# Kernel tuning notes

Measured on AMD Instinct MI355X. Metric: run time of the kernel, lower is better.

## Reference

```python
import jax, jax.numpy as jnp
import numpy as np

B = 64        # BATCH_SIZE
C_IN = 16
L = 8192
FFT0 = 64
FFT1 = 256
CO = 32       # c_out per fft branch (c_out=64 / 2 ffts)
RATIO = FFT1 // FFT0  # 4
EPS = 1e-5


def setup_inputs() -> dict:
    key = jax.random.key(0)
    ks = jax.random.split(key, 12)
    x = jax.random.normal(ks[0], (B, C_IN, L), jnp.float32)
    bn_gamma = 1.0 + 0.1 * jax.random.normal(ks[1], (2, B), jnp.float32)
    bn_beta = 0.1 * jax.random.normal(ks[2], (2, B), jnp.float32)
    mk_r = 0.1 * jax.random.normal(ks[3], (RATIO, RATIO), jnp.float32)
    mk_i = 0.1 * jax.random.normal(ks[4], (RATIO, RATIO), jnp.float32)
    mb_r = 0.1 * jax.random.normal(ks[5], (RATIO,), jnp.float32)
    mb_i = 0.1 * jax.random.normal(ks[6], (RATIO,), jnp.float32)
    fk0_r = 0.1 * jax.random.normal(ks[7], (FFT0 // 2 + 1, C_IN, CO), jnp.float32)
    fk0_i = 0.1 * jax.random.normal(ks[8], (FFT0 // 2 + 1, C_IN, CO), jnp.float32)
    fk1_r = 0.1 * jax.random.normal(ks[9], (FFT1 // 2 + 1, C_IN, CO), jnp.float32)
    fk1_i = 0.1 * jax.random.normal(ks[10], (FFT1 // 2 + 1, C_IN, CO), jnp.float32)
    pbias = 0.1 * jax.random.normal(ks[11], (2 * CO,), jnp.float32)
    return dict(x=x, bn_gamma=bn_gamma, bn_beta=bn_beta, mk_r=mk_r, mk_i=mk_i,
                mb_r=mb_r, mb_i=mb_i, fk0_r=fk0_r, fk0_i=fk0_i,
                fk1_r=fk1_r, fk1_i=fk1_i, pbias=pbias)


def _stft(x2d, n):
    # torch.stft(center=True, pad_mode='reflect', hop=n_fft, rect window),
    # then keep onesided bins and drop the last frame (as in the module).
    N = x2d.shape[0]
    xp = jnp.pad(x2d, ((0, 0), (n // 2, n // 2)), mode='reflect')
    frames = xp.reshape(N, -1, n)               # (N, T+1, n), hop == n_fft
    spec = jnp.fft.rfft(frames, axis=-1)        # onesided == [:, :, :n//2+1]
    return spec[:, :-1, :]                      # drop last frame -> (N, T, n//2+1)


def _zero_interp(p, ratio, out_f):
    # interleave (ratio-1) zeros along the freq axis, then crop to out_f bins
    b, t, f, c = p.shape
    z = jnp.zeros((b, t, f, ratio - 1, c), p.dtype)
    q = jnp.concatenate([p[:, :, :, None, :], z], axis=3).reshape(b, t, f * ratio, c)
    return q[:, :, :out_f, :]


def _cbn(xc, g, b):
    # BatchNorm2d(BATCH_SIZE) after permute(3,0,1,2): channel dim == batch dim,
    # stats over (c_in, T, F) per batch element; complex mean, |.|^2 variance.
    mu = jnp.mean(xc, axis=(1, 2, 3), keepdims=True)
    d = xc - mu
    var = jnp.mean((d * jnp.conj(d)).real, axis=(1, 2, 3), keepdims=True)
    xh = d / jnp.sqrt(var + EPS)
    return xh * g[:, None, None, None] + b[:, None, None, None]


def _istft(out, n):
    # out: (B, T, F, CO) complex. Mirrors permute/reshape + frame repeat + istft
    # (hop=n_fft, rect window, center=True -> trim n//2 on both ends).
    Bq, T, F, Co = out.shape
    pf = out.transpose(0, 3, 2, 1).reshape(Bq * Co, F, T)
    pf = jnp.concatenate([pf, pf[:, :, :1]], axis=-1)   # append copy of frame 0 -> T+1 frames
    fr = jnp.fft.irfft(pf, n=n, axis=1)                 # (N, n, T+1)
    sig = fr.transpose(0, 2, 1).reshape(Bq * Co, -1)    # overlap-add trivial (hop=n)
    sig = sig[:, n // 2: n // 2 + T * n]                # length L
    return sig.reshape(Bq, Co, -1).transpose(0, 2, 1)   # (B, L, CO)


def _forward(x, bn_gamma, bn_beta, mk_r, mk_i, mb_r, mb_i,
             fk0_r, fk0_i, fk1_r, fk1_i, pbias):
    x2 = x.reshape(B * C_IN, L)

    def spec(n):
        s = _stft(x2, n)                                 # (B*C_IN, T, n//2+1)
        T = s.shape[1]
        return s.reshape(B, C_IN, T, n // 2 + 1).transpose(0, 2, 3, 1)  # (B,T,F,C_IN)

    p0 = spec(FFT0)   # (B, 128, 33, 16)
    p1 = spec(FFT1)   # (B, 32, 129, 16)

    # attention merge across time (small fft -> large fft scale)
    pm = p0.reshape(B, -1, RATIO, FFT0 // 2 + 1, C_IN).transpose(0, 1, 3, 4, 2)  # (B,T1,F0,C,r)
    kc = mk_r + 1j * mk_i
    att = jnp.einsum('btfcr,rs->btfcs', pm, kc) + (mb_r + 1j * mb_i)
    a = jax.nn.softmax(jnp.abs(att), axis=-1)            # real weights (complex(a,0) in torch)
    merged = jnp.sum(pm * a, axis=-1) * float(RATIO)     # (B, T1, F0, C_IN)

    F1 = FFT1 // 2 + 1
    mask01 = _zero_interp(jnp.ones(merged.shape, jnp.float32), RATIO, F1)
    up = _zero_interp(merged, RATIO, F1)

    acc0 = p0                                            # own-scale mask is all ones
    acc1 = mask01 * up + (1.0 - mask01) * p1             # cross-scale + complementary mask

    def head(acc, g, b, fkr, fki, n):
        xbn = _cbn(acc, g, b)
        out = jnp.einsum('btfi,fio->btfo', xbn, fkr + 1j * fki)  # FILTER_FLAG merge
        return _istft(out, n)

    t0 = head(acc0, bn_gamma[0], bn_beta[0], fk0_r, fk0_i, FFT0)  # (B, L, CO)
    t1 = head(acc1, bn_gamma[1], bn_beta[1], fk1_r, fk1_i, FFT1)  # (B, L, CO)

    y = jnp.concatenate([t0, t1], axis=2) + pbias        # + patch_bias.real
    y = jax.nn.relu(y)                                   # ACT_DOMAIN == 'time'
    return y.transpose(0, 2, 1)                          # (B, c_out, L)


def reference(x, bn_gamma, bn_beta, mk_r, mk_i, mb_r, mb_i,
              fk0_r, fk0_i, fk1_r, fk1_i, pbias):
    return _forward(x, bn_gamma, bn_beta, mk_r, mk_i, mb_r, mb_i,
                    fk0_r, fk0_i, fk1_r, fk1_i, pbias)
```

## Files before the change

kernel.cpp:

```cpp
#include <hip/hip_runtime.h>
#include <math.h>

#define BB   64
#define CIN  16
#define LL   8192
#define CO   32
#define TCO  64
constexpr int T0n = 128;
constexpr int T1n = 32;
constexpr int F0n = 33;
constexpr int F1n = 129;

typedef unsigned int   uint32;
typedef unsigned short u16;
typedef __attribute__((ext_vector_type(8))) _Float16 half8;
typedef __attribute__((ext_vector_type(4))) float    f32x4;

template<int N, int F, int TFR, int NTILES, int KTT, int MT_W, int NT_W,
         int NT_STRIDE, bool MT_SPLIT>
__global__ __launch_bounds__(256)
void stft_mfma_kernel(const float* __restrict__ x,
                      const u16* __restrict__ dhi, const u16* __restrict__ dlo,
                      float* __restrict__ p) {
    constexpr int PADN = N + 8;
    __shared__ __align__(16) u16 Xhi[TFR * PADN];
    __shared__ __align__(16) u16 Xlo[TFR * PADN];
    int bc = blockIdx.x;
    const float* xrow = x + (size_t)bc * LL;

    for (int i = threadIdx.x; i < TFR * N; i += 256) {
        int row = i / N, colk = i % N;
        int gi = i - N / 2;
        gi = gi < 0 ? -gi : gi;
        float v = xrow[gi];
        _Float16 h = (_Float16)v;
        _Float16 l = (_Float16)(v - (float)h);
        Xhi[row * PADN + colk] = *(u16*)&h;
        Xlo[row * PADN + colk] = *(u16*)&l;
    }
    __syncthreads();

    int lane = threadIdx.x & 63, w = threadIdx.x >> 6;
    int col = lane & 15, quad = lane >> 4;
    f32x4 acc[MT_W][NT_W];
    #pragma unroll
    for (int mi = 0; mi < MT_W; ++mi)
        #pragma unroll
        for (int nj = 0; nj < NT_W; ++nj) {
            f32x4 z = {0.f, 0.f, 0.f, 0.f};
            acc[mi][nj] = z;
        }

    for (int kt = 0; kt < KTT; ++kt) {
        half8 ah[MT_W], al[MT_W];
        #pragma unroll
        for (int mi = 0; mi < MT_W; ++mi) {
            int mt = MT_SPLIT ? (w * MT_W + mi) : mi;
            int t  = mt * 16 + col;
            const u16* base = &Xhi[t * PADN + kt * 32 + quad * 8];
            ah[mi] = *(const half8*)base;
            al[mi] = *(const half8*)&Xlo[t * PADN + kt * 32 + quad * 8];
        }
        #pragma unroll
        for (int nj = 0; nj < NT_W; ++nj) {
            int nt = MT_SPLIT ? nj : (w + nj * NT_STRIDE);
            if (nt < NTILES) {
                half8 bh = ((const half8*)dhi)[(nt * KTT + kt) * 64 + lane];
                half8 bl = ((const half8*)dlo)[(nt * KTT + kt) * 64 + lane];
                #pragma unroll
                for (int mi = 0; mi < MT_W; ++mi) {
                    acc[mi][nj] = __builtin_amdgcn_mfma_f32_16x16x32_f16(ah[mi], bh, acc[mi][nj], 0, 0, 0);
                    acc[mi][nj] = __builtin_amdgcn_mfma_f32_16x16x32_f16(ah[mi], bl, acc[mi][nj], 0, 0, 0);
                    acc[mi][nj] = __builtin_amdgcn_mfma_f32_16x16x32_f16(al[mi], bh, acc[mi][nj], 0, 0, 0);
                }
            }
        }
    }

    int b = bc / CIN, c = bc % CIN;
    #pragma unroll
    for (int mi = 0; mi < MT_W; ++mi) {
        int mt = MT_SPLIT ? (w * MT_W + mi) : mi;
        #pragma unroll
        for (int nj = 0; nj < NT_W; ++nj) {
            int nt = MT_SPLIT ? nj : (w + nj * NT_STRIDE);
            if (nt < NTILES) {
                int j = nt * 16 + col;
                if (j < 2 * F) {
                    int t0 = mt * 16 + quad * 4;
                    f32x4 a = acc[mi][nj];
                    #pragma unroll
                    for (int r = 0; r < 4; ++r) {
                        p[(((size_t)b * TFR + t0 + r) * CIN + c) * (2 * F) + j] = a[r];
                    }
                }
            }
        }
    }
}

__global__ __launch_bounds__(256)
void init_d_kernel(u16* __restrict__ dhi0, u16* __restrict__ dlo0,
                   u16* __restrict__ dhi1, u16* __restrict__ dlo1) {
    int idx = blockIdx.x * 256 + threadIdx.x;
    constexpr int SZ0 = 5 * 2 * 64 * 8;
    constexpr int SZ1 = 17 * 8 * 64 * 8;
    int N, F, KTT, id; u16 *dh, *dl;
    if (idx < SZ0)            { N = 64;  F = F0n; KTT = 2; dh = dhi0; dl = dlo0; id = idx; }
    else if (idx < SZ0 + SZ1) { N = 256; F = F1n; KTT = 8; dh = dhi1; dl = dlo1; id = idx - SZ0; }
    else return;
    int jj   = id & 7;
    int lane = (id >> 3) & 63;
    int rest = id >> 9;
    int kt   = rest % KTT;
    int nt   = rest / KTT;
    int j = nt * 16 + (lane & 15);
    int k = kt * 32 + (lane >> 4) * 8 + jj;
    float v = 0.f;
    if (j < 2 * F) {
        int f = j >> 1;
        int u = (f * k) % N;
        double th = 6.283185307179586476925286766559 * (double)u / (double)N;
        v = (float)((j & 1) ? -sin(th) : cos(th));
    }
    _Float16 h = (_Float16)v;
    _Float16 l = (_Float16)(v - (float)h);
    dh[id] = *(u16*)&h;
    dl[id] = *(u16*)&l;
}

__global__ __launch_bounds__(256)
void merge_kernel(const float2* __restrict__ p0, float2* __restrict__ p1,
                  const float* __restrict__ mkr, const float* __restrict__ mki,
                  const float* __restrict__ mbr, const float* __restrict__ mbi) {
    int idx = blockIdx.x * 256 + threadIdx.x;
    const int total = BB * T1n * CIN * F0n;
    if (idx >= total) return;
    int f0 = idx % F0n; int r1 = idx / F0n;
    int c  = r1 % CIN;  int r2 = r1 / CIN;
    int t1 = r2 % T1n;  int b  = r2 / T1n;
    float2 pm[4];
    #pragma unroll
    for (int r = 0; r < 4; ++r) {
        int t = t1 * 4 + r;
        pm[r] = p0[(((size_t)b * T0n + t) * CIN + c) * F0n + f0];
    }
    float mag[4], mx = -1e30f;
    #pragma unroll
    for (int s = 0; s < 4; ++s) {
        float atr = mbr[s], ati = mbi[s];
        #pragma unroll
        for (int r = 0; r < 4; ++r) {
            float kr = mkr[r * 4 + s], ki = mki[r * 4 + s];
            atr = fmaf(pm[r].x, kr, atr); atr = fmaf(-pm[r].y, ki, atr);
            ati = fmaf(pm[r].x, ki, ati); ati = fmaf(pm[r].y, kr, ati);
        }
        mag[s] = sqrtf(atr * atr + ati * ati);
        mx = fmaxf(mx, mag[s]);
    }
    float se = 0.f;
    #pragma unroll
    for (int s = 0; s < 4; ++s) { mag[s] = expf(mag[s] - mx); se += mag[s]; }
    float inv = 4.0f / se;
    float mr = 0.f, mi = 0.f;
    #pragma unroll
    for (int r = 0; r < 4; ++r) { mr = fmaf(pm[r].x, mag[r], mr); mi = fmaf(pm[r].y, mag[r], mi); }
    p1[(((size_t)b * T1n + t1) * CIN + c) * F1n + 4 * f0] = make_float2(mr * inv, mi * inv);
}

__global__ __launch_bounds__(256)
void cbn_kernel(const float2* __restrict__ p0, const float2* __restrict__ p1,
                const float* __restrict__ gamma, const float* __restrict__ beta,
                float4* __restrict__ bn) {
    int head = blockIdx.x >> 6;
    int b    = blockIdx.x & 63;
    int Nel  = head ? (T1n * CIN * F1n) : (T0n * CIN * F0n);
    const float2* base = head ? (p1 + (size_t)b * (T1n * CIN * F1n))
                              : (p0 + (size_t)b * (T0n * CIN * F0n));
    float sr = 0.f, si = 0.f, s2 = 0.f;
    for (int i = threadIdx.x; i < Nel; i += 256) {
        float2 v = base[i];
        sr += v.x; si += v.y;
        s2 = fmaf(v.x, v.x, s2); s2 = fmaf(v.y, v.y, s2);
    }
    __shared__ float red[3][256];
    red[0][threadIdx.x] = sr; red[1][threadIdx.x] = si; red[2][threadIdx.x] = s2;
    __syncthreads();
    for (int off = 128; off > 0; off >>= 1) {
        if (threadIdx.x < off) {
            red[0][threadIdx.x] += red[0][threadIdx.x + off];
            red[1][threadIdx.x] += red[1][threadIdx.x + off];
            red[2][threadIdx.x] += red[2][threadIdx.x + off];
        }
        __syncthreads();
    }
    if (threadIdx.x == 0) {
        float invN = 1.f / (float)Nel;
        float mur = red[0][0] * invN, mui = red[1][0] * invN;
        float var = red[2][0] * invN - mur * mur - mui * mui;
        float g = gamma[head * BB + b] * rsqrtf(var + 1e-5f);
        bn[head * BB + b] = make_float4(g, beta[head * BB + b] - mur * g, -mui * g, 0.f);
    }
}

__global__ __launch_bounds__(256)
void init_w_kernel(u16* __restrict__ whi0, u16* __restrict__ wlo0,
                   u16* __restrict__ whi1, u16* __restrict__ wlo1) {
    int idx = blockIdx.x * 256 + threadIdx.x;
    int N, F, KT, id; u16 *dh, *dl;
    if (idx < 6144)              { N = 64;  F = F0n; KT = 3; dh = whi0; dl = wlo0; id = idx; }
    else if (idx < 6144 + 73728) { N = 256; F = F1n; KT = 9; dh = whi1; dl = wlo1; id = idx - 6144; }
    else return;
    int j    = id & 7;
    int lane = (id >> 3) & 63;
    int rest = id >> 9;
    int kt   = rest % KT;
    int mt   = rest / KT;
    int m  = mt * 16 + (lane & 15);
    int k2 = kt * 32 + (lane >> 4) * 8 + j;
    float v = 0.f;
    if (k2 < 2 * F) {
        int f = k2 >> 1;
        double scale = (f == 0 || f == F - 1) ? (1024.0 / N) : (2048.0 / N);
        int u = (m * f) % N;
        double th = 6.283185307179586476925286766559 * (double)u / (double)N;
        v = (float)((k2 & 1) ? (-scale * sin(th)) : (scale * cos(th)));
    }
    _Float16 h = (_Float16)v;
    _Float16 l = (_Float16)(v - (float)h);
    dh[id] = *(u16*)&h;
    dl[id] = *(u16*)&l;
}

__global__ __launch_bounds__(256)
void init_fk_kernel(const float* __restrict__ r0, const float* __restrict__ i0,
                    const float* __restrict__ r1, const float* __restrict__ i1,
                    float4* __restrict__ q0, float4* __restrict__ q1,
                    float2* __restrict__ s0, float2* __restrict__ s1) {
    int idx = blockIdx.x * 256 + threadIdx.x;
    constexpr int NQ0 = 8 * F0n * 32;
    constexpr int NQ1 = 8 * F1n * 32;
    constexpr int NS0 = F0n * 32;
    constexpr int NS1 = F1n * 32;
    if (idx < NQ0) {
        int id = idx;
        int c2 = id / (F0n * 32); int rem = id % (F0n * 32);
        int f = rem >> 5, o = rem & 31;
        int s = (f * CIN + 2 * c2) * CO + o;
        q0[id] = make_float4(r0[s], i0[s], r0[s + CO], i0[s + CO]);
    } else if (idx < NQ0 + NQ1) {
        int id = idx - NQ0;
        int c2 = id / (F1n * 32); int rem = id % (F1n * 32);
        int f = rem >> 5, o = rem & 31;
        int s = (f * CIN + 2 * c2) * CO + o;
        q1[id] = make_float4(r1[s], i1[s], r1[s + CO], i1[s + CO]);
    } else if (idx < NQ0 + NQ1 + NS0) {
        int id = idx - NQ0 - NQ1;
        int f = id >> 5, o = id & 31;
        float sr = 0.f, si = 0.f;
        for (int ci = 0; ci < CIN; ++ci) {
            int s = (f * CIN + ci) * CO + o;
            sr += r0[s]; si += i0[s];
        }
        s0[id] = make_float2(sr, si);
    } else if (idx < NQ0 + NQ1 + NS0 + NS1) {
        int id = idx - NQ0 - NQ1 - NS0;
        int f = id >> 5, o = id & 31;
        float sr = 0.f, si = 0.f;
        for (int ci = 0; ci < CIN; ++ci) {
            int s = (f * CIN + ci) * CO + o;
            sr += r1[s]; si += i1[s];
        }
        s1[id] = make_float2(sr, si);
    }
}

template<int N, int F, int TFR, int CH0, int KT, int KPAD>
__global__ __launch_bounds__(256)
void istft_kernel(const float2* __restrict__ p,
                  const u16* __restrict__ whi, const u16* __restrict__ wlo,
                  const float4* __restrict__ fkq, const float2* __restrict__ fks,
                  const float4* __restrict__ bn,
                  const float* __restrict__ pbias, float* __restrict__ out) {
    constexpr int MTW = N / 64;
    constexpr int FCO = F * CO;
    constexpr int QN  = (FCO + 255) / 256;
    __shared__ __align__(16) u16 smem[2][32][KPAD];
    auto& Shi = smem[0];
    auto& Slo = smem[1];
    float2* xs = (float2*)&smem[1][0][0];
    static_assert(CIN * F * 8 <= 32 * KPAD * 2, "scratch fits Slo");

    int t  = blockIdx.x % (TFR + 1);
    int b  = blockIdx.x / (TFR + 1);
    int tf = (t == TFR) ? 0 : t;
    float4 par = bn[(CH0 ? 1 : 0) * BB + b];
    const float2* acc = p + ((size_t)b * TFR + tf) * CIN * F;

    {
        const float4* a4 = (const float4*)acc;
        float4* x4 = (float4*)xs;
        for (int i = threadIdx.x; i < CIN * F / 2; i += 256) x4[i] = a4[i];
    }
    __syncthreads();

    uint32 rlo[QN];
    #pragma unroll
    for (int q = 0; q < QN; ++q) {
        int i = threadIdx.x + q * 256;
        if (i < FCO) {
            int f = i >> 5, o = i & 31;
            float re = 0.f, im = 0.f;
            #pragma unroll
            for (int c2 = 0; c2 < 8; ++c2) {
                float4 kk = fkq[c2 * FCO + i];
                float2 xa = xs[(2 * c2) * F + f];
                float2 xb = xs[(2 * c2 + 1) * F + f];
                re = fmaf(xa.x, kk.x, re); re = fmaf(-xa.y, kk.y, re);
                im = fmaf(xa.x, kk.y, im); im = fmaf(xa.y, kk.x, im);
                re = fmaf(xb.x, kk.z, re); re = fmaf(-xb.y, kk.w, re);
                im = fmaf(xb.x, kk.w, im); im = fmaf(xb.y, kk.z, im);
            }
            float2 fv = fks[i];
            float res = fmaf(par.x, re, fmaf(par.y, fv.x, -par.z * fv.y)) * 32.f;
            float ims = fmaf(par.x, im, fmaf(par.y, fv.y,  par.z * fv.x)) * 32.f;
            _Float16 rh = (_Float16)res; _Float16 rl = (_Float16)(res - (float)rh);
            _Float16 ih = (_Float16)ims; _Float16 il = (_Float16)(ims - (float)ih);
            ((uint32*)&Shi[o][0])[f] = ((uint32)(*(u16*)&ih) << 16) | (uint32)(*(u16*)&rh);
            rlo[q] = ((uint32)(*(u16*)&il) << 16) | (uint32)(*(u16*)&rl);
        }
    }
    __syncthreads();

    #pragma unroll
    for (int q = 0; q < QN; ++q) {
        int i = threadIdx.x + q * 256;
        if (i < FCO) {
            int f = i >> 5, o = i & 31;
            ((uint32*)&Slo[o][0])[f] = rlo[q];
        }
    }
    for (int i = threadIdx.x; i < 32 * (KT * 16 - F); i += 256) {
        constexpr int cols = KT * 16 - F;
        int o = i / cols, j = i - o * cols;
        ((uint32*)&Shi[o][0])[F + j] = 0;
        ((uint32*)&Slo[o][0])[F + j] = 0;
    }
    __syncthreads();

    int lane = threadIdx.x & 63, wave = threadIdx.x >> 6;
    int col = lane & 15, quad = lane >> 4;
    f32x4 accv[MTW][2];
    #pragma unroll
    for (int mt = 0; mt < MTW; ++mt)
        #pragma unroll
        for (int nt = 0; nt < 2; ++nt) {
            f32x4 z = {0.f, 0.f, 0.f, 0.f};
            accv[mt][nt] = z;
        }
    for (int kt = 0; kt < KT; ++kt) {
        half8 wah[MTW], wal[MTW];
        #pragma unroll
        for (int mt = 0; mt < MTW; ++mt) {
            int mtile = wave * MTW + mt;
            wah[mt] = ((const half8*)whi)[(mtile * KT + kt) * 64 + lane];
            wal[mt] = ((const half8*)wlo)[(mtile * KT + kt) * 64 + lane];
        }
        half8 bh0 = *(const half8*)&Shi[col][kt * 32 + quad * 8];
        half8 bh1 = *(const half8*)&Shi[16 + col][kt * 32 + quad * 8];
        half8 bl0 = *(const half8*)&Slo[col][kt * 32 + quad * 8];
        half8 bl1 = *(const half8*)&Slo[16 + col][kt * 32 + quad * 8];
        #pragma unroll
        for (int mt = 0; mt < MTW; ++mt) {
            accv[mt][0] = __builtin_amdgcn_mfma_f32_16x16x32_f16(wah[mt], bh0, accv[mt][0], 0, 0, 0);
            accv[mt][0] = __builtin_amdgcn_mfma_f32_16x16x32_f16(wah[mt], bl0, accv[mt][0], 0, 0, 0);
            accv[mt][0] = __builtin_amdgcn_mfma_f32_16x16x32_f16(wal[mt], bh0, accv[mt][0], 0, 0, 0);
            accv[mt][1] = __builtin_amdgcn_mfma_f32_16x16x32_f16(wah[mt], bh1, accv[mt][1], 0, 0, 0);
            accv[mt][1] = __builtin_amdgcn_mfma_f32_16x16x32_f16(wah[mt], bl1, accv[mt][1], 0, 0, 0);
            accv[mt][1] = __builtin_amdgcn_mfma_f32_16x16x32_f16(wal[mt], bh1, accv[mt][1], 0, 0, 0);
        }
    }
    constexpr float UNSCALE = 1.0f / 32768.0f;
    size_t bb = (size_t)b * TCO;
    #pragma unroll
    for (int mt = 0; mt < MTW; ++mt) {
        int l0 = t * N + (wave * MTW + mt) * 16 + quad * 4 - N / 2;
        if ((unsigned)l0 < LL) {
            #pragma unroll
            for (int nt = 0; nt < 2; ++nt) {
                int ch = CH0 + nt * 16 + col;
                float pb = pbias[ch];
                f32x4 a = accv[mt][nt];
                float4 v;
                v.x = fmaxf(fmaf(a[0], UNSCALE, pb), 0.f);
                v.y = fmaxf(fmaf(a[1], UNSCALE, pb), 0.f);
                v.z = fmaxf(fmaf(a[2], UNSCALE, pb), 0.f);
                v.w = fmaxf(fmaf(a[3], UNSCALE, pb), 0.f);
                *(float4*)(out + (bb + ch) * LL + l0) = v;
            }
        }
    }
}

extern "C" void kernel_launch(void* const* d_in, const int* in_sizes, int n_in,
                              void* d_out, int out_size, void* d_ws, size_t ws_size,
                              hipStream_t stream) {
    const float* x     = (const float*)d_in[0];
    const float* gam   = (const float*)d_in[1];
    const float* bet   = (const float*)d_in[2];
    const float* mkr   = (const float*)d_in[3];
    const float* mki   = (const float*)d_in[4];
    const float* mbr   = (const float*)d_in[5];
    const float* mbi   = (const float*)d_in[6];
    const float* fk0r  = (const float*)d_in[7];
    const float* fk0i  = (const float*)d_in[8];
    const float* fk1r  = (const float*)d_in[9];
    const float* fk1i  = (const float*)d_in[10];
    const float* pbias = (const float*)d_in[11];
    float* out = (float*)d_out;

    float2* p0   = (float2*)d_ws;
    float2* p1   = p0 + (size_t)BB * T0n * CIN * F0n;
    float4* bnp  = (float4*)(p1 + (size_t)BB * T1n * CIN * F1n);
    u16*    whi0 = (u16*)(bnp + 2 * BB);
    u16*    wlo0 = whi0 + 6144;
    u16*    whi1 = wlo0 + 6144;
    u16*    wlo1 = whi1 + 73728;
    float4* fkq0 = (float4*)(wlo1 + 73728);
    float4* fkq1 = fkq0 + 8 * F0n * 32;
    float2* fks0 = (float2*)(fkq1 + 8 * F1n * 32);
    float2* fks1 = fks0 + F0n * 32;
    u16*    dhi0 = (u16*)(fks1 + F1n * 32);
    u16*    dlo0 = dhi0 + 5120;
    u16*    dhi1 = dlo0 + 5120;
    u16*    dlo1 = dhi1 + 69632;

    init_w_kernel<<<(6144 + 73728 + 255) / 256, 256, 0, stream>>>(whi0, wlo0, whi1, wlo1);
    init_d_kernel<<<(5120 + 69632 + 255) / 256, 256, 0, stream>>>(dhi0, dlo0, dhi1, dlo1);
    init_fk_kernel<<<(8 * (F0n + F1n) * 32 + (F0n + F1n) * 32 + 255) / 256, 256, 0, stream>>>(
        fk0r, fk0i, fk1r, fk1i, fkq0, fkq1, fks0, fks1);
    stft_mfma_kernel<64, F0n, 128, 5, 2, 2, 5, 1, true><<<BB * CIN, 256, 0, stream>>>(
        x, dhi0, dlo0, (float*)p0);
    stft_mfma_kernel<256, F1n, 32, 17, 8, 2, 5, 4, false><<<BB * CIN, 256, 0, stream>>>(
        x, dhi1, dlo1, (float*)p1);
    merge_kernel<<<(BB * T1n * CIN * F0n) / 256, 256, 0, stream>>>(p0, p1, mkr, mki, mbr, mbi);
    cbn_kernel<<<128, 256, 0, stream>>>(p0, p1, gam, bet, bnp);
    istft_kernel<64, 33, 128, 0, 3, 104><<<BB * (T0n + 1), 256, 0, stream>>>(
        p0, whi0, wlo0, fkq0, fks0, bnp, pbias, out);
    istft_kernel<256, 129, 32, 32, 9, 296><<<BB * (T1n + 1), 256, 0, stream>>>(
        p1, whi1, wlo1, fkq1, fks1, bnp, pbias, out);
}
```

Measured before the change: 451.9 us.

## Split iSTFT into batched einsum kernel and half-size symmetric irfft MFMA kernel

Each per-frame istft kernel is split into two kernels. An einsum kernel processes a group of frames per block, so the filter weights loaded into registers are reused across G frames, and it writes the complex spectra to a workspace buffer. A separate irfft kernel then exploits the symmetry between the first and second half of each output frame: it computes only half the inverse-DFT matrix rows and gets the other half by flipping the sign of odd frequency bins in the B operand. This halves the weight matrix and its loads. In exchange it adds a global round trip for the intermediate spectra and one extra kernel launch per head.

```diff
diff --git a/kernel.cpp b/kernel.cpp
--- a/kernel.cpp
+++ b/kernel.cpp
@@ -15,6 +15,17 @@
 typedef unsigned short u16;
 typedef __attribute__((ext_vector_type(8))) _Float16 half8;
 typedef __attribute__((ext_vector_type(4))) float    f32x4;
+typedef __attribute__((ext_vector_type(4))) uint32   u32x4;
+
+__device__ inline half8 flip_pm(half8 v) {
+    u32x4 u;
+    __builtin_memcpy(&u, &v, 16);
+    u.y ^= 0x80008000u;
+    u.w ^= 0x80008000u;
+    half8 r;
+    __builtin_memcpy(&r, &u, 16);
+    return r;
+}
 
 template<int N, int F, int TFR, int NTILES, int KTT, int MT_W, int NT_W,
          int NT_STRIDE, bool MT_SPLIT>
@@ -57,8 +68,7 @@
         for (int mi = 0; mi < MT_W; ++mi) {
             int mt = MT_SPLIT ? (w * MT_W + mi) : mi;
             int t  = mt * 16 + col;
-            const u16* base = &Xhi[t * PADN + kt * 32 + quad * 8];
-            ah[mi] = *(const half8*)base;
+            ah[mi] = *(const half8*)&Xhi[t * PADN + kt * 32 + quad * 8];
             al[mi] = *(const half8*)&Xlo[t * PADN + kt * 32 + quad * 8];
         }
         #pragma unroll
@@ -207,9 +217,11 @@
 void init_w_kernel(u16* __restrict__ whi0, u16* __restrict__ wlo0,
                    u16* __restrict__ whi1, u16* __restrict__ wlo1) {
     int idx = blockIdx.x * 256 + threadIdx.x;
+    constexpr int SZ0 = 2 * 3 * 64 * 8;
+    constexpr int SZ1 = 8 * 9 * 64 * 8;
     int N, F, KT, id; u16 *dh, *dl;
-    if (idx < 6144)              { N = 64;  F = F0n; KT = 3; dh = whi0; dl = wlo0; id = idx; }
-    else if (idx < 6144 + 73728) { N = 256; F = F1n; KT = 9; dh = whi1; dl = wlo1; id = idx - 6144; }
+    if (idx < SZ0)            { N = 64;  F = F0n; KT = 3; dh = whi0; dl = wlo0; id = idx; }
+    else if (idx < SZ0 + SZ1) { N = 256; F = F1n; KT = 9; dh = whi1; dl = wlo1; id = idx - SZ0; }
     else return;
     int j    = id & 7;
     int lane = (id >> 3) & 63;
@@ -275,70 +287,71 @@
     }
 }
 
-template<int N, int F, int TFR, int CH0, int KT, int KPAD>
-__global__ __launch_bounds__(256)
-void istft_kernel(const float2* __restrict__ p,
+template<int F, int TFR, int CH0, int G>
+__global__ __launch_bounds__(256)
+void einsum_kernel(const float2* __restrict__ p, const float4* __restrict__ fkq,
+                   const float2* __restrict__ fks, const float4* __restrict__ bn,
+                   float2* __restrict__ S) {
+    constexpr int FCO = F * 32;
+    constexpr int NG  = TFR / G;
+    __shared__ float2 xs[G][CIN * F];
+    int grp = blockIdx.x % NG, b = blockIdx.x / NG;
+    float4 par = bn[(CH0 ? 1 : 0) * BB + b];
+    {
+        const float4* a4 = (const float4*)(p + ((size_t)b * TFR + grp * G) * CIN * F);
+        float4* x4 = (float4*)&xs[0][0];
+        for (int i = threadIdx.x; i < G * CIN * F / 2; i += 256) x4[i] = a4[i];
+    }
+    __syncthreads();
+    float2* Sg = S + ((size_t)b * TFR + (size_t)grp * G) * FCO;
+    for (int i = threadIdx.x; i < FCO; i += 256) {
+        int f = i >> 5;
+        float4 kk[8];
+        #pragma unroll
+        for (int c2 = 0; c2 < 8; ++c2) kk[c2] = fkq[c2 * FCO + i];
+        float2 fv = fks[i];
+        float base_re = fmaf(par.y, fv.x, -par.z * fv.y);
+        float base_im = fmaf(par.y, fv.y,  par.z * fv.x);
+        #pragma unroll 4
+        for (int g = 0; g < G; ++g) {
+            float re = 0.f, im = 0.f;
+            #pragma unroll
+            for (int c2 = 0; c2 < 8; ++c2) {
+                float2 xa = xs[g][(2 * c2) * F + f];
+                float2 xb = xs[g][(2 * c2 + 1) * F + f];
+                float4 kkc = kk[c2];
+                re = fmaf(xa.x, kkc.x, re); re = fmaf(-xa.y, kkc.y, re);
+                im = fmaf(xa.x, kkc.y, im); im = fmaf(xa.y, kkc.x, im);
+                re = fmaf(xb.x, kkc.z, re); re = fmaf(-xb.y, kkc.w, re);
+                im = fmaf(xb.x, kkc.w, im); im = fmaf(xb.y, kkc.z, im);
+            }
+            Sg[(size_t)g * FCO + i] = make_float2(
+                fmaf(par.x, re, base_re) * 32.f,
+                fmaf(par.x, im, base_im) * 32.f);
+        }
+    }
+}
+
+template<int N, int F, int TFR, int CH0, int KT, int KPAD, int WBT, bool NTSPLIT>
+__global__ __launch_bounds__(256)
+void irfft_kernel(const float2* __restrict__ S,
                   const u16* __restrict__ whi, const u16* __restrict__ wlo,
-                  const float4* __restrict__ fkq, const float2* __restrict__ fks,
-                  const float4* __restrict__ bn,
                   const float* __restrict__ pbias, float* __restrict__ out) {
-    constexpr int MTW = N / 64;
-    constexpr int FCO = F * CO;
-    constexpr int QN  = (FCO + 255) / 256;
-    __shared__ __align__(16) u16 smem[2][32][KPAD];
-    auto& Shi = smem[0];
-    auto& Slo = smem[1];
-    float2* xs = (float2*)&smem[1][0][0];
-    static_assert(CIN * F * 8 <= 32 * KPAD * 2, "scratch fits Slo");
-
+    constexpr int FCO = F * 32;
+    constexpr int WNT = NTSPLIT ? 1 : 2;
+    __shared__ __align__(16) u16 Shi[32][KPAD];
+    __shared__ __align__(16) u16 Slo[32][KPAD];
     int t  = blockIdx.x % (TFR + 1);
     int b  = blockIdx.x / (TFR + 1);
     int tf = (t == TFR) ? 0 : t;
-    float4 par = bn[(CH0 ? 1 : 0) * BB + b];
-    const float2* acc = p + ((size_t)b * TFR + tf) * CIN * F;
-
-    {
-        const float4* a4 = (const float4*)acc;
-        float4* x4 = (float4*)xs;
-        for (int i = threadIdx.x; i < CIN * F / 2; i += 256) x4[i] = a4[i];
-    }
-    __syncthreads();
-
-    uint32 rlo[QN];
-    #pragma unroll
-    for (int q = 0; q < QN; ++q) {
-        int i = threadIdx.x + q * 256;
-        if (i < FCO) {
-            int f = i >> 5, o = i & 31;
-            float re = 0.f, im = 0.f;
-            #pragma unroll
-            for (int c2 = 0; c2 < 8; ++c2) {
-                float4 kk = fkq[c2 * FCO + i];
-                float2 xa = xs[(2 * c2) * F + f];
-                float2 xb = xs[(2 * c2 + 1) * F + f];
-                re = fmaf(xa.x, kk.x, re); re = fmaf(-xa.y, kk.y, re);
-                im = fmaf(xa.x, kk.y, im); im = fmaf(xa.y, kk.x, im);
-                re = fmaf(xb.x, kk.z, re); re = fmaf(-xb.y, kk.w, re);
-                im = fmaf(xb.x, kk.w, im); im = fmaf(xb.y, kk.z, im);
-            }
-            float2 fv = fks[i];
-            float res = fmaf(par.x, re, fmaf(par.y, fv.x, -par.z * fv.y)) * 32.f;
-            float ims = fmaf(par.x, im, fmaf(par.y, fv.y,  par.z * fv.x)) * 32.f;
-            _Float16 rh = (_Float16)res; _Float16 rl = (_Float16)(res - (float)rh);
-            _Float16 ih = (_Float16)ims; _Float16 il = (_Float16)(ims - (float)ih);
-            ((uint32*)&Shi[o][0])[f] = ((uint32)(*(u16*)&ih) << 16) | (uint32)(*(u16*)&rh);
-            rlo[q] = ((uint32)(*(u16*)&il) << 16) | (uint32)(*(u16*)&rl);
-        }
-    }
-    __syncthreads();
-
-    #pragma unroll
-    for (int q = 0; q < QN; ++q) {
-        int i = threadIdx.x + q * 256;
-        if (i < FCO) {
-            int f = i >> 5, o = i & 31;
-            ((uint32*)&Slo[o][0])[f] = rlo[q];
-        }
+    const float2* src = S + ((size_t)b * TFR + tf) * FCO;
+    for (int i = threadIdx.x; i < FCO; i += 256) {
+        float2 v = src[i];
+        int f = i >> 5, o = i & 31;
+        _Float16 rh = (_Float16)v.x; _Float16 rl = (_Float16)(v.x - (float)rh);
+        _Float16 ih = (_Float16)v.y; _Float16 il = (_Float16)(v.y - (float)ih);
+        ((uint32*)&Shi[o][0])[f] = ((uint32)(*(u16*)&ih) << 16) | (uint32)(*(u16*)&rh);
+        ((uint32*)&Slo[o][0])[f] = ((uint32)(*(u16*)&il) << 16) | (uint32)(*(u16*)&rl);
     }
     for (int i = threadIdx.x; i < 32 * (KT * 16 - F); i += 256) {
         constexpr int cols = KT * 16 - F;
@@ -348,55 +361,65 @@
     }
     __syncthreads();
 
-    int lane = threadIdx.x & 63, wave = threadIdx.x >> 6;
+    int lane = threadIdx.x & 63, w = threadIdx.x >> 6;
     int col = lane & 15, quad = lane >> 4;
-    f32x4 accv[MTW][2];
-    #pragma unroll
-    for (int mt = 0; mt < MTW; ++mt)
-        #pragma unroll
-        for (int nt = 0; nt < 2; ++nt) {
+    f32x4 accB[WBT][WNT], accD[WBT][WNT];
+    #pragma unroll
+    for (int mi = 0; mi < WBT; ++mi)
+        #pragma unroll
+        for (int nj = 0; nj < WNT; ++nj) {
             f32x4 z = {0.f, 0.f, 0.f, 0.f};
-            accv[mt][nt] = z;
+            accB[mi][nj] = z; accD[mi][nj] = z;
         }
     for (int kt = 0; kt < KT; ++kt) {
-        half8 wah[MTW], wal[MTW];
-        #pragma unroll
-        for (int mt = 0; mt < MTW; ++mt) {
-            int mtile = wave * MTW + mt;
-            wah[mt] = ((const half8*)whi)[(mtile * KT + kt) * 64 + lane];
-            wal[mt] = ((const half8*)wlo)[(mtile * KT + kt) * 64 + lane];
-        }
-        half8 bh0 = *(const half8*)&Shi[col][kt * 32 + quad * 8];
-        half8 bh1 = *(const half8*)&Shi[16 + col][kt * 32 + quad * 8];
-        half8 bl0 = *(const half8*)&Slo[col][kt * 32 + quad * 8];
-        half8 bl1 = *(const half8*)&Slo[16 + col][kt * 32 + quad * 8];
-        #pragma unroll
-        for (int mt = 0; mt < MTW; ++mt) {
-            accv[mt][0] = __builtin_amdgcn_mfma_f32_16x16x32_f16(wah[mt], bh0, accv[mt][0], 0, 0, 0);
-            accv[mt][0] = __builtin_amdgcn_mfma_f32_16x16x32_f16(wah[mt], bl0, accv[mt][0], 0, 0, 0);
-            accv[mt][0] = __builtin_amdgcn_mfma_f32_16x16x32_f16(wal[mt], bh0, accv[mt][0], 0, 0, 0);
-            accv[mt][1] = __builtin_amdgcn_mfma_f32_16x16x32_f16(wah[mt], bh1, accv[mt][1], 0, 0, 0);
-            accv[mt][1] = __builtin_amdgcn_mfma_f32_16x16x32_f16(wah[mt], bl1, accv[mt][1], 0, 0, 0);
-            accv[mt][1] = __builtin_amdgcn_mfma_f32_16x16x32_f16(wal[mt], bh1, accv[mt][1], 0, 0, 0);
+        half8 bh[WNT], bl[WNT], bhm[WNT], blm[WNT];
+        #pragma unroll
+        for (int nj = 0; nj < WNT; ++nj) {
+            int nt = NTSPLIT ? (w & 1) : nj;
+            bh[nj]  = *(const half8*)&Shi[nt * 16 + col][kt * 32 + quad * 8];
+            bl[nj]  = *(const half8*)&Slo[nt * 16 + col][kt * 32 + quad * 8];
+            bhm[nj] = flip_pm(bh[nj]);
+            blm[nj] = flip_pm(bl[nj]);
+        }
+        #pragma unroll
+        for (int mi = 0; mi < WBT; ++mi) {
+            int mt = NTSPLIT ? (w >> 1) : (w * WBT + mi);
+            half8 ah = ((const half8*)whi)[(mt * KT + kt) * 64 + lane];
+            half8 al = ((const half8*)wlo)[(mt * KT + kt) * 64 + lane];
+            #pragma unroll
+            for (int nj = 0; nj < WNT; ++nj) {
+                accB[mi][nj] = __builtin_amdgcn_mfma_f32_16x16x32_f16(ah, bh[nj],  accB[mi][nj], 0, 0, 0);
+                accB[mi][nj] = __builtin_amdgcn_mfma_f32_16x16x32_f16(ah, bl[nj],  accB[mi][nj], 0, 0, 0);
+                accB[mi][nj] = __builtin_amdgcn_mfma_f32_16x16x32_f16(al, bh[nj],  accB[mi][nj], 0, 0, 0);
+                accD[mi][nj] = __builtin_amdgcn_mfma_f32_16x16x32_f16(ah, bhm[nj], accD[mi][nj], 0, 0, 0);
+                accD[mi][nj] = __builtin_amdgcn_mfma_f32_16x16x32_f16(ah, blm[nj], accD[mi][nj], 0, 0, 0);
+                accD[mi][nj] = __builtin_amdgcn_mfma_f32_16x16x32_f16(al, bhm[nj], accD[mi][nj], 0, 0, 0);
+            }
         }
     }
     constexpr float UNSCALE = 1.0f / 32768.0f;
     size_t bb = (size_t)b * TCO;
     #pragma unroll
-    for (int mt = 0; mt < MTW; ++mt) {
-        int l0 = t * N + (wave * MTW + mt) * 16 + quad * 4 - N / 2;
-        if ((unsigned)l0 < LL) {
-            #pragma unroll
-            for (int nt = 0; nt < 2; ++nt) {
-                int ch = CH0 + nt * 16 + col;
-                float pb = pbias[ch];
-                f32x4 a = accv[mt][nt];
-                float4 v;
-                v.x = fmaxf(fmaf(a[0], UNSCALE, pb), 0.f);
-                v.y = fmaxf(fmaf(a[1], UNSCALE, pb), 0.f);
-                v.z = fmaxf(fmaf(a[2], UNSCALE, pb), 0.f);
-                v.w = fmaxf(fmaf(a[3], UNSCALE, pb), 0.f);
-                *(float4*)(out + (bb + ch) * LL + l0) = v;
+    for (int mi = 0; mi < WBT; ++mi) {
+        int mt = NTSPLIT ? (w >> 1) : (w * WBT + mi);
+        #pragma unroll
+        for (int hh = 0; hh < 2; ++hh) {
+            int m  = mt * 16 + quad * 4 + hh * (N / 2);
+            int l0 = t * N + m - N / 2;
+            if ((unsigned)l0 < LL) {
+                #pragma unroll
+                for (int nj = 0; nj < WNT; ++nj) {
+                    int nt = NTSPLIT ? (w & 1) : nj;
+                    int ch = CH0 + nt * 16 + col;
+                    float pb = pbias[ch];
+                    f32x4 a = hh ? accD[mi][nj] : accB[mi][nj];
+                    float4 v;
+                    v.x = fmaxf(fmaf(a[0], UNSCALE, pb), 0.f);
+                    v.y = fmaxf(fmaf(a[1], UNSCALE, pb), 0.f);
+                    v.z = fmaxf(fmaf(a[2], UNSCALE, pb), 0.f);
+                    v.w = fmaxf(fmaf(a[3], UNSCALE, pb), 0.f);
+                    *(float4*)(out + (bb + ch) * LL + l0) = v;
+                }
             }
         }
     }
@@ -422,20 +445,21 @@
     float2* p0   = (float2*)d_ws;
     float2* p1   = p0 + (size_t)BB * T0n * CIN * F0n;
     float4* bnp  = (float4*)(p1 + (size_t)BB * T1n * CIN * F1n);
-    u16*    whi0 = (u16*)(bnp + 2 * BB);
-    u16*    wlo0 = whi0 + 6144;
-    u16*    whi1 = wlo0 + 6144;
-    u16*    wlo1 = whi1 + 73728;
-    float4* fkq0 = (float4*)(wlo1 + 73728);
+    float4* fkq0 = bnp + 2 * BB;
     float4* fkq1 = fkq0 + 8 * F0n * 32;
     float2* fks0 = (float2*)(fkq1 + 8 * F1n * 32);
     float2* fks1 = fks0 + F0n * 32;
-    u16*    dhi0 = (u16*)(fks1 + F1n * 32);
+    float2* Sbuf = fks1 + F1n * 32;
+    u16*    whi0 = (u16*)(Sbuf + (size_t)BB * T0n * F0n * 32);
+    u16*    wlo0 = whi0 + 3072;
+    u16*    whi1 = wlo0 + 3072;
+    u16*    wlo1 = whi1 + 36864;
+    u16*    dhi0 = wlo1 + 36864;
     u16*    dlo0 = dhi0 + 5120;
     u16*    dhi1 = dlo0 + 5120;
     u16*    dlo1 = dhi1 + 69632;
 
-    init_w_kernel<<<(6144 + 73728 + 255) / 256, 256, 0, stream>>>(whi0, wlo0, whi1, wlo1);
+    init_w_kernel<<<(3072 + 36864 + 255) / 256, 256, 0, stream>>>(whi0, wlo0, whi1, wlo1);
     init_d_kernel<<<(5120 + 69632 + 255) / 256, 256, 0, stream>>>(dhi0, dlo0, dhi1, dlo1);
     init_fk_kernel<<<(8 * (F0n + F1n) * 32 + (F0n + F1n) * 32 + 255) / 256, 256, 0, stream>>>(
         fk0r, fk0i, fk1r, fk1i, fkq0, fkq1, fks0, fks1);
@@ -445,8 +469,12 @@
         x, dhi1, dlo1, (float*)p1);
     merge_kernel<<<(BB * T1n * CIN * F0n) / 256, 256, 0, stream>>>(p0, p1, mkr, mki, mbr, mbi);
     cbn_kernel<<<128, 256, 0, stream>>>(p0, p1, gam, bet, bnp);
-    istft_kernel<64, 33, 128, 0, 3, 104><<<BB * (T0n + 1), 256, 0, stream>>>(
-        p0, whi0, wlo0, fkq0, fks0, bnp, pbias, out);
-    istft_kernel<256, 129, 32, 32, 9, 296><<<BB * (T1n + 1), 256, 0, stream>>>(
-        p1, whi1, wlo1, fkq1, fks1, bnp, pbias, out);
-}
+    einsum_kernel<F1n, T1n, 32, 4><<<BB * (T1n / 4), 256, 0, stream>>>(
+        p1, fkq1, fks1, bnp, Sbuf);
+    irfft_kernel<256, F1n, T1n, 32, 9, 296, 2, false><<<BB * (T1n + 1), 256, 0, stream>>>(
+        Sbuf, whi1, wlo1, pbias, out);
+    einsum_kernel<F0n, T0n, 0, 16><<<BB * (T0n / 16), 256, 0, stream>>>(
+        p0, fkq0, fks0, bnp, Sbuf);
+    irfft_kernel<64, F0n, T0n, 0, 3, 104, 1, true><<<BB * (T0n + 1), 256, 0, stream>>>(
+        Sbuf, whi0, wlo0, pbias, out);
+}
```

New measurement: 467.8 us. +3.5%, slower.
